# Kernel optimization log

Hardware: AMD Instinct MI355X
Metric: run time of the kernel (lower is better)

Reference implementation:

```python
import jax, jax.numpy as jnp
import numpy as np

N_NODES = 100000
IN_FEATURES = 5000
OUT_FEATURES = 64
NNZ = 4000000


def setup_inputs() -> dict:
    key = jax.random.key(0)
    k_row, k_col, k_val, k_w, k_b = jax.random.split(key, 5)
    rows = jax.random.randint(k_row, (NNZ,), 0, N_NODES, dtype=jnp.int64 if jax.config.jax_enable_x64 else jnp.int32)
    cols = jax.random.randint(k_col, (NNZ,), 0, IN_FEATURES, dtype=rows.dtype)
    index = jnp.stack([rows, cols], axis=0)  # [2, nnz] COO
    value = jax.random.uniform(k_val, (NNZ,), dtype=jnp.float32)
    # kaiming_uniform_(mode='fan_out', a=sqrt(5)) on [in, out]: fan_out = out_features
    gain = np.sqrt(2.0 / (1.0 + 5.0))
    bound_w = gain * np.sqrt(3.0 / OUT_FEATURES)
    weight = jax.random.uniform(k_w, (IN_FEATURES, OUT_FEATURES), jnp.float32, -bound_w, bound_w)
    bound_b = 1.0 / np.sqrt(OUT_FEATURES)
    bias = jax.random.uniform(k_b, (OUT_FEATURES,), jnp.float32, -bound_b, bound_b)
    return {"index": index, "value": value, "n": N_NODES, "weight": weight, "bias": bias}


def reference(index, value, n, weight, bias):
    # spmm: out[r, :] = sum over nnz with row==r of value * weight[col, :]
    rows, cols = index[0], index[1]
    contrib = value[:, None] * weight[cols]            # [nnz, out] gather + scale
    res = jax.ops.segment_sum(contrib, rows, num_segments=n)  # [n, out] scatter-add
    return res + bias[None, :]
```

## Files before the change

kernel.cpp:

```cpp
#include <hip/hip_runtime.h>


#define NBF 1024
#define DMAX 128
#define CH 4096
#define CC 1536
#define SP_T 512

__global__ void k_zero1024(int* __restrict__ p) { p[threadIdx.x] = 0; }

__global__ void k_ghist(const int* __restrict__ rows, int nnz, unsigned M, int S,
                        int* __restrict__ gcnt) {
    __shared__ int h[NBF];
    int t = threadIdx.x;
    for (int i = t; i < NBF; i += blockDim.x) h[i] = 0;
    __syncthreads();
    for (int i = blockIdx.x * blockDim.x + t; i < nnz; i += gridDim.x * blockDim.x) {
        unsigned r = (unsigned)rows[i];
        int f = (int)(((unsigned long long)r * M) >> S);
        atomicAdd(&h[f], 1);
    }
    __syncthreads();
    for (int i = t; i < NBF; i += blockDim.x)
        if (h[i]) atomicAdd(&gcnt[i], h[i]);
}

__global__ __launch_bounds__(1024) void kB_off(const int* __restrict__ gcnt,
        const int* __restrict__ hist2dC, int nChunks, int* __restrict__ fineBase,
        int* __restrict__ cursorF, int* __restrict__ blockOffC, int doOff) {
    __shared__ int sE[NBF];
    __shared__ int wsum[16];
    __shared__ int totalSh;
    int t = threadIdx.x, lane = t & 63, wv = t >> 6;
    int v = gcnt[t];
    int x = v;
#pragma unroll
    for (int off = 1; off < 64; off <<= 1) {
        int y = __shfl_up(x, off, 64);
        if (lane >= off) x += y;
    }
    if (lane == 63) wsum[wv] = x;
    __syncthreads();
    if (t < 16) {
        int s = wsum[t], xs = s;
#pragma unroll
        for (int off = 1; off < 16; off <<= 1) {
            int y = __shfl_up(xs, off, 16);
            if (t >= off) xs += y;
        }
        wsum[t] = xs - s;
    }
    __syncthreads();
    int incl = x + wsum[wv], excl = incl - v;
    sE[t] = excl;
    if (blockIdx.x == 0) {
        fineBase[t] = excl;
        cursorF[t] = excl;
        if (t == NBF - 1) fineBase[NBF] = incl;
    }
    __syncthreads();
    if (!doOff) return;
    int c = blockIdx.x;
    int carry = sE[c << 4];
    for (int b2 = 0; b2 < nChunks; b2 += 1024) {
        int idx = b2 + t;
        int hv = (idx < nChunks) ? hist2dC[(idx << 6) + c] : 0;
        int hx = hv;
#pragma unroll
        for (int off = 1; off < 64; off <<= 1) {
            int y = __shfl_up(hx, off, 64);
            if (lane >= off) hx += y;
        }
        if (lane == 63) wsum[wv] = hx;
        __syncthreads();
        if (t < 16) {
            int s = wsum[t], xs = s;
#pragma unroll
            for (int off = 1; off < 16; off <<= 1) {
                int y = __shfl_up(xs, off, 16);
                if (t >= off) xs += y;
            }
            wsum[t] = xs - s;
        }
        __syncthreads();
        int hincl = hx + wsum[wv];
        if (idx < nChunks) blockOffC[(idx << 6) + c] = carry + hincl - hv;
        if (t == 1023) totalSh = hincl;
        __syncthreads();
        carry += totalSh;
    }
}

__global__ __launch_bounds__(1024) void k_bin_direct(const int* __restrict__ rows,
        const int* __restrict__ cols, const float* __restrict__ vals, int nnz,
        unsigned M, int S, int d, int* __restrict__ cursorF,
        unsigned long long* __restrict__ pairs1) {
    __shared__ unsigned long long stage[CH];
    __shared__ int histF[NBF], scF[NBF], adjF[NBF];
    __shared__ int wsum[16];
    int t = threadIdx.x, lane = t & 63, wv = t >> 6;
    long long base = (long long)blockIdx.x * CH;
    int count = (int)min((long long)CH, (long long)nnz - base);
    histF[t] = 0;
    __syncthreads();
    int f4[4], rk4[4];
    unsigned long long pk4[4];
#pragma unroll
    for (int k = 0; k < 4; ++k) {
        int i = t + (k << 10);
        f4[k] = -1;
        if (i < count) {
            unsigned r = (unsigned)rows[base + i];
            int c = cols[base + i];
            float vv = vals[base + i];
            int f = (int)(((unsigned long long)r * M) >> S);
            int lr = (int)r - f * d;
            f4[k] = f;
            rk4[k] = atomicAdd(&histF[f], 1);
            pk4[k] = ((unsigned long long)__float_as_uint(vv) << 32) |
                     ((unsigned)f << 20) | ((unsigned)lr << 13) | (unsigned)c;
        }
    }
    __syncthreads();
    int v = histF[t], x = v;
#pragma unroll
    for (int off = 1; off < 64; off <<= 1) {
        int y = __shfl_up(x, off, 64);
        if (lane >= off) x += y;
    }
    if (lane == 63) wsum[wv] = x;
    __syncthreads();
    if (t < 16) {
        int s = wsum[t], xs = s;
#pragma unroll
        for (int off = 1; off < 16; off <<= 1) {
            int y = __shfl_up(xs, off, 16);
            if (t >= off) xs += y;
        }
        wsum[t] = xs - s;
    }
    __syncthreads();
    int incl = x + wsum[wv];
    scF[t] = incl;
    if (v > 0) {
        int g = atomicAdd(&cursorF[t], v);
        adjF[t] = g - (incl - v);
    }
    __syncthreads();
#pragma unroll
    for (int k = 0; k < 4; ++k)
        if (f4[k] >= 0) stage[(scF[f4[k]] - histF[f4[k]]) + rk4[k]] = pk4[k];
    __syncthreads();
    for (int i = t; i < count; i += 1024) {
        unsigned long long p = stage[i];
        int f = (int)((p >> 20) & 1023);
        pairs1[adjF[f] + i] = p;
    }
}

__global__ __launch_bounds__(SP_T, 8) void k_spmm5(
        const unsigned long long* __restrict__ pairs, const int* __restrict__ fineBase,
        const float* __restrict__ weight, const float* __restrict__ bias,
        float* __restrict__ out, int d, int n) {
    __shared__ unsigned long long stage[CC];
    __shared__ int histR[DMAX], scR[DMAX];
    extern __shared__ float acc[];
    int b = blockIdx.x, t = threadIdx.x;
    int row0 = b * d;
    if (row0 >= n) return;
    int nrows = min(d, n - row0);
    int start = fineBase[b], end = fineBase[b + 1];

    for (int i = t; i < (nrows << 6); i += SP_T) acc[i] = 0.0f;

    int g = t >> 4, fq = t & 15;
    for (int cb = start; cb < end; cb += CC) {
        int cnt = min(CC, end - cb);
        if (t < DMAX) histR[t] = 0;
        __syncthreads();
        int lr3[3], rk3[3];
        unsigned long long pk3[3];
#pragma unroll
        for (int k = 0; k < 3; ++k) {
            int i = t + (k << 9);
            lr3[k] = -1;
            if (i < cnt) {
                unsigned long long p = pairs[cb + i];
                int lr = (int)((p >> 13) & 127);
                lr3[k] = lr;
                rk3[k] = atomicAdd(&histR[lr], 1);
                pk3[k] = p;
            }
        }
        __syncthreads();
        if (t < DMAX) {
            int v = histR[t], x = v;
            int lane = t & 63;
#pragma unroll
            for (int off = 1; off < 64; off <<= 1) {
                int y = __shfl_up(x, off, 64);
                if (lane >= off) x += y;
            }
            scR[t] = x;
        }
        __syncthreads();
        if (t >= 64 && t < DMAX) scR[t] += scR[63];
        __syncthreads();
#pragma unroll
        for (int k = 0; k < 3; ++k)
            if (lr3[k] >= 0) stage[(scR[lr3[k]] - histR[lr3[k]]) + rk3[k]] = pk3[k];
        __syncthreads();

        for (int r = g; r < nrows; r += 32) {
            int e = scR[r], s = e - histR[r];
            if (s >= e) continue;
            float4 a = {0.0f, 0.0f, 0.0f, 0.0f};
            int j = s;
            for (; j + 4 <= e; j += 4) {
                unsigned long long p0 = stage[j + 0];
                unsigned long long p1 = stage[j + 1];
                unsigned long long p2 = stage[j + 2];
                unsigned long long p3 = stage[j + 3];
                const float4 w0 = *(const float4*)(weight + (((int)(p0 & 8191)) << 6) + (fq << 2));
                const float4 w1 = *(const float4*)(weight + (((int)(p1 & 8191)) << 6) + (fq << 2));
                const float4 w2 = *(const float4*)(weight + (((int)(p2 & 8191)) << 6) + (fq << 2));
                const float4 w3 = *(const float4*)(weight + (((int)(p3 & 8191)) << 6) + (fq << 2));
                float v0 = __uint_as_float((unsigned)(p0 >> 32));
                float v1 = __uint_as_float((unsigned)(p1 >> 32));
                float v2 = __uint_as_float((unsigned)(p2 >> 32));
                float v3 = __uint_as_float((unsigned)(p3 >> 32));
                a.x = fmaf(v0, w0.x, a.x); a.y = fmaf(v0, w0.y, a.y);
                a.z = fmaf(v0, w0.z, a.z); a.w = fmaf(v0, w0.w, a.w);
                a.x = fmaf(v1, w1.x, a.x); a.y = fmaf(v1, w1.y, a.y);
                a.z = fmaf(v1, w1.z, a.z); a.w = fmaf(v1, w1.w, a.w);
                a.x = fmaf(v2, w2.x, a.x); a.y = fmaf(v2, w2.y, a.y);
                a.z = fmaf(v2, w2.z, a.z); a.w = fmaf(v2, w2.w, a.w);
                a.x = fmaf(v3, w3.x, a.x); a.y = fmaf(v3, w3.y, a.y);
                a.z = fmaf(v3, w3.z, a.z); a.w = fmaf(v3, w3.w, a.w);
            }
            for (; j < e; ++j) {
                unsigned long long p = stage[j];
                float vv = __uint_as_float((unsigned)(p >> 32));
                const float4 w = *(const float4*)(weight + (((int)(p & 8191)) << 6) + (fq << 2));
                a.x = fmaf(vv, w.x, a.x); a.y = fmaf(vv, w.y, a.y);
                a.z = fmaf(vv, w.z, a.z); a.w = fmaf(vv, w.w, a.w);
            }
            float4* ap = (float4*)&acc[(r << 6) + (fq << 2)];
            float4 o = *ap;
            o.x += a.x; o.y += a.y; o.z += a.z; o.w += a.w;
            *ap = o;
        }
        __syncthreads();
    }

    for (int i = t; i < (nrows << 6); i += SP_T)
        out[((long long)row0 << 6) + i] = acc[i] + bias[i & 63];
}

extern "C" void kernel_launch(void* const* d_in, const int* in_sizes, int n_in,
                              void* d_out, int out_size, void* d_ws, size_t ws_size,
                              hipStream_t stream) {
    const int*   index  = (const int*)d_in[0];
    const float* value  = (const float*)d_in[1];
    const float* weight = (const float*)d_in[3];
    const float* bias   = (const float*)d_in[4];
    float*       out    = (float*)d_out;

    int nnz = in_sizes[0] / 2;
    int n   = out_size / 64;
    const int* rows = index;
    const int* cols = index + nnz;

    int d = (n + NBF - 1) / NBF;
    unsigned M = 0;
    int S = 0;
    for (S = 20; S <= 40; ++S) {
        unsigned long long m = ((1ull << S) + (unsigned)d - 1) / (unsigned)d;
        unsigned long long e = m * (unsigned long long)d - (1ull << S);
        if (m <= 0xffffffffull && e * (unsigned long long)(n > 0 ? n - 1 : 0) < (1ull << S)) {
            M = (unsigned)m;
            break;
        }
    }

    int nChunks = (nnz + CH - 1) / CH;
    char* ws = (char*)d_ws;
    int* fineBase = (int*)ws;
    int* cursorF  = (int*)(ws + (8 << 10));
    int* gcnt     = (int*)(ws + (12 << 10));
    size_t offC = 64 << 10;
    size_t szC  = (((size_t)nChunks * 64 * 4) + 255) & ~(size_t)255;
    size_t offO = offC + szC;
    size_t offF = offO + szC;
    size_t szF  = (((size_t)nChunks * NBF * 4) + 255) & ~(size_t)255;
    size_t offP1 = offF + szF;
    size_t szP   = (((size_t)nnz * 8) + 255) & ~(size_t)255;
    int* hist2dC   = (int*)(ws + offC);
    int* blockOffC = (int*)(ws + offO);
    unsigned long long* pairs1 = (unsigned long long*)(ws + offP1);
    unsigned long long* pairs3 = (unsigned long long*)(ws + offC);

    bool fits = ws_size >= offP1 + szP;
    unsigned long long* pairs = fits ? pairs1 : pairs3;

    k_zero1024<<<1, 1024, 0, stream>>>(gcnt);
    size_t smem = (size_t)d * 64 * sizeof(float);
    k_ghist<<<256, 512, 0, stream>>>(rows, nnz, M, S, gcnt);
    kB_off<<<1, 1024, 0, stream>>>(gcnt, hist2dC, nChunks, fineBase, cursorF,
                                   blockOffC, 0);
    k_bin_direct<<<nChunks, 1024, 0, stream>>>(rows, cols, value, nnz, M, S, d,
                                               cursorF, pairs);
    k_spmm5<<<NBF, SP_T, smem, stream>>>(pairs, fineBase, weight, bias, out, d, n);
}
```

Measured before the change: 195.6 us.

## Replace histogram pass with fixed-capacity bins and double-buffer SpMM staging

Drops the global row histogram and prefix-scan kernels. Each coarse bin now gets a fixed number of slots in the workspace, and pairs that do not fit spill to an overflow buffer that the SpMM kernel folds in with LDS float atomics. The SpMM kernel also double-buffers its staging chunks, so the next chunk's global loads and local sort overlap with the gather-FMA on the current one. This removes two launches and one full read of the row indices, at the cost of depending on workspace size and a serial overflow scan that every block reads when bins overflow.

```diff
diff --git a/kernel.cpp b/kernel.cpp
--- a/kernel.cpp
+++ b/kernel.cpp
@@ -4,97 +4,24 @@
 #define NBF 1024
 #define DMAX 128
 #define CH 4096
-#define CC 1536
+#define CC2 768
 #define SP_T 512
 
-__global__ void k_zero1024(int* __restrict__ p) { p[threadIdx.x] = 0; }
-
-__global__ void k_ghist(const int* __restrict__ rows, int nnz, unsigned M, int S,
-                        int* __restrict__ gcnt) {
-    __shared__ int h[NBF];
-    int t = threadIdx.x;
-    for (int i = t; i < NBF; i += blockDim.x) h[i] = 0;
-    __syncthreads();
-    for (int i = blockIdx.x * blockDim.x + t; i < nnz; i += gridDim.x * blockDim.x) {
-        unsigned r = (unsigned)rows[i];
-        int f = (int)(((unsigned long long)r * M) >> S);
-        atomicAdd(&h[f], 1);
-    }
-    __syncthreads();
-    for (int i = t; i < NBF; i += blockDim.x)
-        if (h[i]) atomicAdd(&gcnt[i], h[i]);
-}
-
-__global__ __launch_bounds__(1024) void kB_off(const int* __restrict__ gcnt,
-        const int* __restrict__ hist2dC, int nChunks, int* __restrict__ fineBase,
-        int* __restrict__ cursorF, int* __restrict__ blockOffC, int doOff) {
-    __shared__ int sE[NBF];
-    __shared__ int wsum[16];
-    __shared__ int totalSh;
-    int t = threadIdx.x, lane = t & 63, wv = t >> 6;
-    int v = gcnt[t];
-    int x = v;
-#pragma unroll
-    for (int off = 1; off < 64; off <<= 1) {
-        int y = __shfl_up(x, off, 64);
-        if (lane >= off) x += y;
-    }
-    if (lane == 63) wsum[wv] = x;
-    __syncthreads();
-    if (t < 16) {
-        int s = wsum[t], xs = s;
-#pragma unroll
-        for (int off = 1; off < 16; off <<= 1) {
-            int y = __shfl_up(xs, off, 16);
-            if (t >= off) xs += y;
-        }
-        wsum[t] = xs - s;
-    }
-    __syncthreads();
-    int incl = x + wsum[wv], excl = incl - v;
-    sE[t] = excl;
-    if (blockIdx.x == 0) {
-        fineBase[t] = excl;
-        cursorF[t] = excl;
-        if (t == NBF - 1) fineBase[NBF] = incl;
-    }
-    __syncthreads();
-    if (!doOff) return;
-    int c = blockIdx.x;
-    int carry = sE[c << 4];
-    for (int b2 = 0; b2 < nChunks; b2 += 1024) {
-        int idx = b2 + t;
-        int hv = (idx < nChunks) ? hist2dC[(idx << 6) + c] : 0;
-        int hx = hv;
-#pragma unroll
-        for (int off = 1; off < 64; off <<= 1) {
-            int y = __shfl_up(hx, off, 64);
-            if (lane >= off) hx += y;
-        }
-        if (lane == 63) wsum[wv] = hx;
-        __syncthreads();
-        if (t < 16) {
-            int s = wsum[t], xs = s;
-#pragma unroll
-            for (int off = 1; off < 16; off <<= 1) {
-                int y = __shfl_up(xs, off, 16);
-                if (t >= off) xs += y;
-            }
-            wsum[t] = xs - s;
-        }
-        __syncthreads();
-        int hincl = hx + wsum[wv];
-        if (idx < nChunks) blockOffC[(idx << 6) + c] = carry + hincl - hv;
-        if (t == 1023) totalSh = hincl;
-        __syncthreads();
-        carry += totalSh;
-    }
-}
-
-__global__ __launch_bounds__(1024) void k_bin_direct(const int* __restrict__ rows,
+__device__ __forceinline__ void ds_fadd(float* p, float v) {
+    unsigned a = (unsigned)(unsigned long long)p;
+    asm volatile("ds_add_f32 %0, %1" :: "v"(a), "v"(v) : "memory");
+}
+
+__global__ void k_init(int* __restrict__ cursorF, int* __restrict__ ovfCnt, int slots) {
+    cursorF[threadIdx.x] = threadIdx.x * slots;
+    if (threadIdx.x == 0) *ovfCnt = 0;
+}
+
+__global__ __launch_bounds__(1024) void k_bin_fixed(const int* __restrict__ rows,
         const int* __restrict__ cols, const float* __restrict__ vals, int nnz,
-        unsigned M, int S, int d, int* __restrict__ cursorF,
-        unsigned long long* __restrict__ pairs1) {
+        unsigned M, int S, int d, int slots, int* __restrict__ cursorF,
+        unsigned long long* __restrict__ pairs1, int* __restrict__ ovfCnt,
+        unsigned long long* __restrict__ ovf) {
     __shared__ unsigned long long stage[CH];
     __shared__ int histF[NBF], scF[NBF], adjF[NBF];
     __shared__ int wsum[16];
@@ -154,73 +81,105 @@
     for (int i = t; i < count; i += 1024) {
         unsigned long long p = stage[i];
         int f = (int)((p >> 20) & 1023);
-        pairs1[adjF[f] + i] = p;
-    }
-}
-
-__global__ __launch_bounds__(SP_T, 8) void k_spmm5(
-        const unsigned long long* __restrict__ pairs, const int* __restrict__ fineBase,
+        int dest = adjF[f] + i;
+        if (dest < (f + 1) * slots) pairs1[dest] = p;
+        else ovf[atomicAdd(ovfCnt, 1)] = p;
+    }
+}
+
+__global__ __launch_bounds__(SP_T, 8) void k_spmm8(
+        const unsigned long long* __restrict__ pairs, const int* __restrict__ cursorF,
+        const int* __restrict__ ovfCnt, const unsigned long long* __restrict__ ovf,
         const float* __restrict__ weight, const float* __restrict__ bias,
-        float* __restrict__ out, int d, int n) {
-    __shared__ unsigned long long stage[CC];
-    __shared__ int histR[DMAX], scR[DMAX];
+        float* __restrict__ out, int d, int n, int slots) {
+    __shared__ unsigned long long stg[2][CC2];
+    __shared__ int histR[2][DMAX], scR[2][DMAX];
     extern __shared__ float acc[];
     int b = blockIdx.x, t = threadIdx.x;
     int row0 = b * d;
     if (row0 >= n) return;
     int nrows = min(d, n - row0);
-    int start = fineBase[b], end = fineBase[b + 1];
+    long long sbase = (long long)b * slots;
+    int cnt = cursorF[b] - (int)sbase;
+    if (cnt > slots) cnt = slots;
+    if (cnt < 0) cnt = 0;
 
     for (int i = t; i < (nrows << 6); i += SP_T) acc[i] = 0.0f;
-
     int g = t >> 4, fq = t & 15;
-    for (int cb = start; cb < end; cb += CC) {
-        int cnt = min(CC, end - cb);
-        if (t < DMAX) histR[t] = 0;
-        __syncthreads();
-        int lr3[3], rk3[3];
-        unsigned long long pk3[3];
-#pragma unroll
-        for (int k = 0; k < 3; ++k) {
+    int nt = (cnt + CC2 - 1) / CC2;
+
+    int lr2[2], rk2[2];
+    unsigned long long pk2[2];
+
+    if (t < DMAX) { histR[0][t] = 0; histR[1][t] = 0; }
+    __syncthreads();
+    if (nt > 0) {
+        int c0 = min(CC2, cnt);
+#pragma unroll
+        for (int k = 0; k < 2; ++k) {
             int i = t + (k << 9);
-            lr3[k] = -1;
-            if (i < cnt) {
-                unsigned long long p = pairs[cb + i];
+            lr2[k] = -1;
+            if (i < c0) {
+                unsigned long long p = pairs[sbase + i];
                 int lr = (int)((p >> 13) & 127);
-                lr3[k] = lr;
-                rk3[k] = atomicAdd(&histR[lr], 1);
-                pk3[k] = p;
-            }
-        }
-        __syncthreads();
-        if (t < DMAX) {
-            int v = histR[t], x = v;
-            int lane = t & 63;
+                lr2[k] = lr; rk2[k] = atomicAdd(&histR[0][lr], 1); pk2[k] = p;
+            }
+        }
+        __syncthreads();
+        if (t < 64) {
+            int v0 = histR[0][t], v1 = histR[0][t + 64];
+            int x0 = v0;
 #pragma unroll
             for (int off = 1; off < 64; off <<= 1) {
-                int y = __shfl_up(x, off, 64);
-                if (lane >= off) x += y;
-            }
-            scR[t] = x;
-        }
-        __syncthreads();
-        if (t >= 64 && t < DMAX) scR[t] += scR[63];
-        __syncthreads();
-#pragma unroll
-        for (int k = 0; k < 3; ++k)
-            if (lr3[k] >= 0) stage[(scR[lr3[k]] - histR[lr3[k]]) + rk3[k]] = pk3[k];
-        __syncthreads();
-
+                int y = __shfl_up(x0, off, 64);
+                if (t >= off) x0 += y;
+            }
+            int tot = __shfl(x0, 63, 64);
+            int x1 = v1;
+#pragma unroll
+            for (int off = 1; off < 64; off <<= 1) {
+                int y = __shfl_up(x1, off, 64);
+                if (t >= off) x1 += y;
+            }
+            x1 += tot;
+            scR[0][t] = x0; scR[0][t + 64] = x1;
+        }
+        __syncthreads();
+#pragma unroll
+        for (int k = 0; k < 2; ++k)
+            if (lr2[k] >= 0) stg[0][scR[0][lr2[k]] - histR[0][lr2[k]] + rk2[k]] = pk2[k];
+        __syncthreads();
+    }
+
+    for (int c = 0; c < nt; ++c) {
+        int cur = c & 1, nxt = cur ^ 1;
+        bool more = (c + 1 < nt);
+        if (more) {
+            int nb = (c + 1) * CC2;
+            int ncnt = min(CC2, cnt - nb);
+#pragma unroll
+            for (int k = 0; k < 2; ++k) {
+                int i = t + (k << 9);
+                lr2[k] = -1;
+                if (i < ncnt) {
+                    unsigned long long p = pairs[sbase + nb + i];
+                    int lr = (int)((p >> 13) & 127);
+                    lr2[k] = lr; rk2[k] = atomicAdd(&histR[nxt][lr], 1); pk2[k] = p;
+                }
+            }
+        } else {
+            lr2[0] = lr2[1] = -1;
+        }
         for (int r = g; r < nrows; r += 32) {
-            int e = scR[r], s = e - histR[r];
+            int e = scR[cur][r], s = e - histR[cur][r];
             if (s >= e) continue;
             float4 a = {0.0f, 0.0f, 0.0f, 0.0f};
             int j = s;
             for (; j + 4 <= e; j += 4) {
-                unsigned long long p0 = stage[j + 0];
-                unsigned long long p1 = stage[j + 1];
-                unsigned long long p2 = stage[j + 2];
-                unsigned long long p3 = stage[j + 3];
+                unsigned long long p0 = stg[cur][j + 0];
+                unsigned long long p1 = stg[cur][j + 1];
+                unsigned long long p2 = stg[cur][j + 2];
+                unsigned long long p3 = stg[cur][j + 3];
                 const float4 w0 = *(const float4*)(weight + (((int)(p0 & 8191)) << 6) + (fq << 2));
                 const float4 w1 = *(const float4*)(weight + (((int)(p1 & 8191)) << 6) + (fq << 2));
                 const float4 w2 = *(const float4*)(weight + (((int)(p2 & 8191)) << 6) + (fq << 2));
@@ -239,7 +198,7 @@
                 a.z = fmaf(v3, w3.z, a.z); a.w = fmaf(v3, w3.w, a.w);
             }
             for (; j < e; ++j) {
-                unsigned long long p = stage[j];
+                unsigned long long p = stg[cur][j];
                 float vv = __uint_as_float((unsigned)(p >> 32));
                 const float4 w = *(const float4*)(weight + (((int)(p & 8191)) << 6) + (fq << 2));
                 a.x = fmaf(vv, w.x, a.x); a.y = fmaf(vv, w.y, a.y);
@@ -251,7 +210,51 @@
             *ap = o;
         }
         __syncthreads();
-    }
+        if (more && t < 64) {
+            int v0 = histR[nxt][t], v1 = histR[nxt][t + 64];
+            int x0 = v0;
+#pragma unroll
+            for (int off = 1; off < 64; off <<= 1) {
+                int y = __shfl_up(x0, off, 64);
+                if (t >= off) x0 += y;
+            }
+            int tot = __shfl(x0, 63, 64);
+            int x1 = v1;
+#pragma unroll
+            for (int off = 1; off < 64; off <<= 1) {
+                int y = __shfl_up(x1, off, 64);
+                if (t >= off) x1 += y;
+            }
+            x1 += tot;
+            scR[nxt][t] = x0; scR[nxt][t + 64] = x1;
+        }
+        __syncthreads();
+#pragma unroll
+        for (int k = 0; k < 2; ++k)
+            if (lr2[k] >= 0) stg[nxt][scR[nxt][lr2[k]] - histR[nxt][lr2[k]] + rk2[k]] = pk2[k];
+        if (t < DMAX) histR[cur][t] = 0;
+        __syncthreads();
+    }
+
+    int oc = *ovfCnt;
+    if (oc > 0) {
+        __syncthreads();
+        for (int i = g; i < oc; i += (SP_T >> 4)) {
+            unsigned long long p = ovf[i];
+            if ((int)((p >> 20) & 1023) == b) {
+                int lr = (int)((p >> 13) & 127);
+                int cc = (int)(p & 8191);
+                float vv = __uint_as_float((unsigned)(p >> 32));
+                const float4 w = *(const float4*)(weight + (cc << 6) + (fq << 2));
+                float* ap = &acc[(lr << 6) + (fq << 2)];
+                ds_fadd(ap + 0, vv * w.x); ds_fadd(ap + 1, vv * w.y);
+                ds_fadd(ap + 2, vv * w.z); ds_fadd(ap + 3, vv * w.w);
+            }
+        }
+        asm volatile("s_waitcnt lgkmcnt(0)" ::: "memory");
+        __builtin_amdgcn_sched_barrier(0);
+    }
+    __syncthreads();
 
     for (int i = t; i < (nrows << 6); i += SP_T)
         out[((long long)row0 << 6) + i] = acc[i] + bias[i & 63];
@@ -285,30 +288,22 @@
 
     int nChunks = (nnz + CH - 1) / CH;
     char* ws = (char*)d_ws;
-    int* fineBase = (int*)ws;
-    int* cursorF  = (int*)(ws + (8 << 10));
-    int* gcnt     = (int*)(ws + (12 << 10));
-    size_t offC = 64 << 10;
-    size_t szC  = (((size_t)nChunks * 64 * 4) + 255) & ~(size_t)255;
-    size_t offO = offC + szC;
-    size_t offF = offO + szC;
-    size_t szF  = (((size_t)nChunks * NBF * 4) + 255) & ~(size_t)255;
-    size_t offP1 = offF + szF;
-    size_t szP   = (((size_t)nnz * 8) + 255) & ~(size_t)255;
-    int* hist2dC   = (int*)(ws + offC);
-    int* blockOffC = (int*)(ws + offO);
-    unsigned long long* pairs1 = (unsigned long long*)(ws + offP1);
-    unsigned long long* pairs3 = (unsigned long long*)(ws + offC);
-
-    bool fits = ws_size >= offP1 + szP;
-    unsigned long long* pairs = fits ? pairs1 : pairs3;
-
-    k_zero1024<<<1, 1024, 0, stream>>>(gcnt);
+    int* cursorF = (int*)ws;
+    int* ovfCnt  = (int*)(ws + 4096);
+    unsigned long long* pairsS = (unsigned long long*)(ws + 65536);
+
+    size_t szOvf = (((size_t)nnz * 8) + 255) & ~(size_t)255;
+    size_t availS = (ws_size > 65536 + szOvf) ? (ws_size - 65536 - szOvf) : 0;
+    long long slotsL = (long long)(availS / ((size_t)NBF * 8));
+    int slots = (int)(slotsL > 6144 ? 6144 : slotsL);
+    if (slots > 64) slots &= ~63;
+    if (slots < 1) slots = 1;
+    unsigned long long* ovf = (unsigned long long*)(ws + 65536 + (size_t)slots * NBF * 8);
+
+    k_init<<<1, 1024, 0, stream>>>(cursorF, ovfCnt, slots);
+    k_bin_fixed<<<nChunks, 1024, 0, stream>>>(rows, cols, value, nnz, M, S, d, slots,
+                                              cursorF, pairsS, ovfCnt, ovf);
     size_t smem = (size_t)d * 64 * sizeof(float);
-    k_ghist<<<256, 512, 0, stream>>>(rows, nnz, M, S, gcnt);
-    kB_off<<<1, 1024, 0, stream>>>(gcnt, hist2dC, nChunks, fineBase, cursorF,
-                                   blockOffC, 0);
-    k_bin_direct<<<nChunks, 1024, 0, stream>>>(rows, cols, value, nnz, M, S, d,
-                                               cursorF, pairs);
-    k_spmm5<<<NBF, SP_T, smem, stream>>>(pairs, fineBase, weight, bias, out, d, n);
-}
+    k_spmm8<<<NBF, SP_T, smem, stream>>>(pairsS, cursorF, ovfCnt, ovf, weight, bias,
+                                         out, d, n, slots);
+}
```

Measured after the change: 185.1 us. 1.06x faster.
